# Optimization experiments

Measured on AMD Instinct MI355X. Metric: run time of the kernel, lower is better.

The kernel has to match this reference:

```python
import jax, jax.numpy as jnp
import numpy as np

# ---- static problem constants ----
B, N, L = 8, 256, 15.0          # molecules, atoms per molecule, cubic cell length (Angstrom)
DL, SIGMA = 1.5, 1.0            # Ewald k-space spacing and Gaussian smearing width
ELEMENTS = np.array([1, 6, 7, 8])
NORM_FACTOR = (1.0 / 90.0474) ** 0.5
TWO_PI = 2.0 * np.pi
KSQ_MAX = (TWO_PI / DL) ** 2
NMAX = int(np.ceil(L / DL))     # 10 -> (2*10+1)^3 = 9261 k-vectors
_g = np.arange(-NMAX, NMAX + 1)
K_GRID = jnp.asarray(np.stack(np.meshgrid(_g, _g, _g, indexing='ij'), -1)
                     .reshape(-1, 3).astype(np.float32))  # [K,3] integer k indices
_zmap = np.full(int(ELEMENTS.max()) + 1, -1)
for _i, _z in enumerate(ELEMENTS):
    _zmap[_z] = _i
Z_INDEX_MAP = jnp.asarray(_zmap)


def setup_inputs() -> dict:
    key = jax.random.key(0)
    k1, k2, k3, k4 = jax.random.split(key, 4)
    positions = jax.random.uniform(k1, (B * N, 3), jnp.float32) * L
    cell = jnp.tile((L * jnp.eye(3, dtype=jnp.float32))[None], (B, 1, 1))
    chi = jax.random.normal(k2, (B * N,), jnp.float32)
    idx = jax.random.randint(k3, (B * N,), 0, len(ELEMENTS))
    atomic_numbers = jnp.asarray(ELEMENTS)[idx]
    batch = jnp.repeat(jnp.arange(B), N)
    J_raw = jax.random.uniform(k4, (len(ELEMENTS),), jnp.float32, 0.5, 1.5)
    system_charge = jnp.zeros((B,), jnp.float32)
    return dict(positions=positions, cell=cell, chi=chi, J_raw=J_raw,
                system_charge=system_charge, atomic_numbers=atomic_numbers, batch=batch)


def _a_matrix(r, cell):
    """Reciprocal-space Ewald interaction matrix A (energy = 0.5 q^T A q), one molecule."""
    recip = TWO_PI * jnp.linalg.inv(cell).T            # rows: reciprocal lattice vectors
    k = K_GRID @ recip                                 # [K,3]
    k2 = jnp.sum(k * k, axis=-1)                       # [K]
    valid = (k2 > 1e-10) & (k2 < KSQ_MAX)
    f = jnp.where(valid, jnp.exp(-0.5 * SIGMA * SIGMA * k2) / jnp.maximum(k2, 1e-10), 0.0)
    vol = jnp.abs(jnp.linalg.det(cell))
    kr = r @ k.T                                       # [N,K]
    c, s = jnp.cos(kr), jnp.sin(kr)
    # A_ij = (4*pi/V) sum_k f(k) cos(k.(r_i - r_j))
    A = (2.0 * TWO_PI / vol) * ((c * f) @ c.T + (s * f) @ s.T)
    # remove Gaussian self-interaction: E_self = -sum_i q_i^2 / (sigma*sqrt(2*pi))
    A = A - (2.0 / (SIGMA * np.sqrt(TWO_PI))) * jnp.eye(N, dtype=r.dtype)
    return A


def _solve_qeq(A, chi_m, J_i, Q):
    """Charge-equilibration with Lagrange multiplier for total-charge constraint."""
    coeffs = jnp.ones((N + 1, N + 1), A.dtype)
    coeffs = coeffs.at[:N, :N].set(A + jnp.diag(J_i))
    coeffs = coeffs.at[N, N].set(0.0)
    rhs = jnp.concatenate([-chi_m, (Q / NORM_FACTOR)[None].astype(A.dtype)])
    sol = jnp.linalg.solve(coeffs, rhs)
    q = sol[:N]
    e = 0.5 * q @ (A @ q)
    return q, e


def reference(positions, cell, chi, J_raw, system_charge, atomic_numbers, batch):
    r = positions.reshape(B, N, 3)
    chi_b = chi.reshape(B, N)
    J_elem = jnp.square(J_raw)
    J_i = J_elem[Z_INDEX_MAP[atomic_numbers]].reshape(B, N)
    A = jax.vmap(_a_matrix)(r, cell)                   # [B,N,N]
    q, e = jax.vmap(_solve_qeq)(A, chi_b, J_i, system_charge)
    all_q_eq = q.reshape(B * N, 1)
    all_ewald = e                                      # [B]
    return all_q_eq, all_ewald
```

## Files before the change

### kernel.cpp

```cpp
#include <hip/hip_runtime.h>
#include <math.h>

#define NBATCH 8
#define NATOM  256
#define NP1    257
#define WROW   258
#define TOTALK 9261
#define KCAP   2560
#define KC     16
#define NB     16
#define UBW    244
#define BDF    768
#define BDB    256

#define TWO_PI_D 6.283185307179586
#define DIAG_SUB 0.7978845608028654

__device__ __constant__ int TI10[10] = {0,0,0,0,1,1,1,2,2,3};
__device__ __constant__ int TJ10[10] = {0,1,2,3,1,2,3,2,3,3};

struct GemmSh {
  int4   kn[KC];
  double kw[KC];
  double cI[KC][64], sI[KC][64];
  double cJ[KC][64], sJ[KC][64];
};

__device__ __forceinline__ void atomAddD(double* p, double v) {
#if defined(__has_builtin)
#if __has_builtin(__builtin_amdgcn_global_atomic_fadd_f64)
  __builtin_amdgcn_global_atomic_fadd_f64(p, v);
  return;
#endif
#endif
  unsigned long long* u = (unsigned long long*)p;
  unsigned long long old = *u, assumed;
  do {
    assumed = old;
    old = atomicCAS(u, assumed,
                    (unsigned long long)__double_as_longlong(
                        v + __longlong_as_double((long long)assumed)));
  } while (old != assumed);
}

__device__ __forceinline__ void classify2(const void* c0, const void* c1, const void* c2,
                                          const float*& chi, const int*& znum)
{
  const void* cands[3] = {c0, c1, c2};
  int got = 0;
  for (int i = 0; i < 3; i++) {
    unsigned uu = ((const unsigned*)cands[i])[0];
    if (uu == 0u) continue;
    else if (uu < 16u) { znum = (const int*)cands[i]; got |= 1; }
    else               { chi  = (const float*)cands[i]; got |= 2; }
  }
  if (got != 3) { chi = (const float*)c0; znum = (const int*)c1; }
}

__global__ __launch_bounds__(256) void zero_planes(
    double* __restrict__ P0g, int nplanes)
{
  const size_t npair = (size_t)nplanes * NBATCH * ((NP1*WROW) >> 1);
  double2* Z = (double2*)P0g;
  const double2 z = make_double2(0.0, 0.0);
  for (size_t i = (size_t)blockIdx.x*256 + threadIdx.x; i < npair;
       i += (size_t)gridDim.x*256)
    Z[i] = z;
}

__global__ __launch_bounds__(256) void prep(
    const float* __restrict__ pos, const float* __restrict__ cell,
    double2* __restrict__ Tg, int4* __restrict__ klist,
    double* __restrict__ kw, int* __restrict__ kcount,
    const void* __restrict__ c0, const void* __restrict__ c1, const void* __restrict__ c2,
    const float* __restrict__ syschg,
    double* __restrict__ P0g, int nplanes)
{
  const int b = blockIdx.x;
  const int tid = threadIdx.x;
  __shared__ double ivs[9];
  __shared__ double prefs;
  __shared__ int cnt;
  if (tid == 0) {
    double c[9];
#pragma unroll
    for (int i = 0; i < 9; i++) c[i] = (double)cell[b*9+i];
    double det = c[0]*(c[4]*c[8]-c[5]*c[7]) - c[1]*(c[3]*c[8]-c[5]*c[6])
               + c[2]*(c[3]*c[7]-c[4]*c[6]);
    double idet = 1.0/det;
    ivs[0]=(c[4]*c[8]-c[5]*c[7])*idet; ivs[1]=(c[2]*c[7]-c[1]*c[8])*idet; ivs[2]=(c[1]*c[5]-c[2]*c[4])*idet;
    ivs[3]=(c[5]*c[6]-c[3]*c[8])*idet; ivs[4]=(c[0]*c[8]-c[2]*c[6])*idet; ivs[5]=(c[2]*c[3]-c[0]*c[5])*idet;
    ivs[6]=(c[3]*c[7]-c[4]*c[6])*idet; ivs[7]=(c[1]*c[6]-c[0]*c[7])*idet; ivs[8]=(c[0]*c[4]-c[1]*c[3])*idet;
    prefs = 2.0*TWO_PI_D/fabs(det);
    cnt = 0;
  }
  __syncthreads();
  {
    const int a = tid;
    double x = (double)pos[((size_t)b*NATOM+a)*3+0];
    double y = (double)pos[((size_t)b*NATOM+a)*3+1];
    double z = (double)pos[((size_t)b*NATOM+a)*3+2];
    double u[3];
    u[0] = TWO_PI_D*(ivs[0]*x + ivs[3]*y + ivs[6]*z);
    u[1] = TWO_PI_D*(ivs[1]*x + ivs[4]*y + ivs[7]*z);
    u[2] = TWO_PI_D*(ivs[2]*x + ivs[5]*y + ivs[8]*z);
#pragma unroll
    for (int d = 0; d < 3; d++) {
      double2* T = Tg + (size_t)((b*3 + d)*21)*256;
      double c1 = cos(u[d]);
      double s1 = sin(u[d]);
      T[10*256 + a] = make_double2(1.0, 0.0);
      T[11*256 + a] = make_double2(c1,  s1);
      T[ 9*256 + a] = make_double2(c1, -s1);
      double cp = c1, sp = s1;
      for (int n = 2; n <= 10; n++) {
        double cn = cp*c1 - sp*s1;
        double sn = sp*c1 + cp*s1;
        cp = cn; sp = sn;
        T[(10+n)*256 + a] = make_double2(cp,  sp);
        T[(10-n)*256 + a] = make_double2(cp, -sp);
      }
    }
  }
  const double ksqmax = (TWO_PI_D/1.5)*(TWO_PI_D/1.5);
  for (int m = tid; m < TOTALK; m += 256) {
    int n1 = m/441 - 10;
    int n2 = (m/21)%21 - 10;
    int n3 = m%21 - 10;
    bool half = (n1 > 0) || (n1 == 0 && (n2 > 0 || (n2 == 0 && n3 > 0)));
    if (!half) continue;
    double d1 = n1, d2 = n2, d3 = n3;
    double kx = TWO_PI_D*(ivs[0]*d1 + ivs[1]*d2 + ivs[2]*d3);
    double ky = TWO_PI_D*(ivs[3]*d1 + ivs[4]*d2 + ivs[5]*d3);
    double kz = TWO_PI_D*(ivs[6]*d1 + ivs[7]*d2 + ivs[8]*d3);
    double k2 = kx*kx + ky*ky + kz*kz;
    if (k2 > 1e-10 && k2 < ksqmax) {
      double w = 2.0 * prefs * exp(-0.5*k2) / k2;
      int slot = atomicAdd(&cnt, 1);
      klist[b*KCAP + slot] = make_int4(n1, n2, n3, 0);
      kw[b*KCAP + slot] = w;
    }
  }
  __syncthreads();
  {
    const float* chi = nullptr; const int* znum = nullptr;
    classify2(c0, c1, c2, chi, znum);
    double* P0b = P0g + (size_t)b*NP1*WROW;
    for (int i = tid; i < NATOM; i += 256) {
      P0b[(size_t)NATOM*WROW + i] = 1.0;
      P0b[(size_t)i*WROW + NATOM] = 1.0;
      P0b[(size_t)i*WROW + 257]   = -(double)chi[b*NATOM + i];
    }
    if (tid == 0) {
      P0b[(size_t)NATOM*WROW + NATOM] = 0.0;
      P0b[(size_t)NATOM*WROW + 257]   = (double)syschg[b]*sqrt(90.0474);
      kcount[b] = cnt;
    }
  }
}

__device__ void gemm_tile(int b, int ti, int tj, int tid,
                          const double2* __restrict__ Tg,
                          const int4* __restrict__ klist,
                          const double* __restrict__ kw, int ks, int ke,
                          double* __restrict__ Ab, bool mirror, GemmSh& S)
{
  const int tx = tid & 15, ty = tid >> 4;
  const int ro = ty << 2, co = tx << 2;
  double acc[16];
#pragma unroll
  for (int i = 0; i < 16; i++) acc[i] = 0.0;

  for (int k0 = ks; k0 < ke; k0 += KC) {
    if (tid < KC) {
      int kk = k0 + tid;
      if (kk < ke) { S.kn[tid] = klist[b*KCAP + kk]; S.kw[tid] = kw[b*KCAP + kk]; }
      else         { S.kn[tid] = make_int4(0,0,0,0); S.kw[tid] = 0.0; }
    }
    __syncthreads();
#pragma unroll
    for (int p = 0; p < 8; p++) {
      int idx = p*256 + tid;
      int a    = idx & 63;
      int kk   = (idx >> 6) & (KC-1);
      int side = idx >> 10;
      int atom = ((side == 0) ? ti : tj) + a;
      int4 nn = S.kn[kk];
      double2 t1 = Tg[(size_t)((b*3+0)*21 + (nn.x+10))*256 + atom];
      double2 t2 = Tg[(size_t)((b*3+1)*21 + (nn.y+10))*256 + atom];
      double2 t3 = Tg[(size_t)((b*3+2)*21 + (nn.z+10))*256 + atom];
      double ex = t1.x*t2.x - t1.y*t2.y;
      double ey = t1.x*t2.y + t1.y*t2.x;
      double cx = ex*t3.x - ey*t3.y;
      double cy = ex*t3.y + ey*t3.x;
      if (side == 0) { double w = S.kw[kk]; S.cI[kk][a] = w*cx; S.sI[kk][a] = w*cy; }
      else           { S.cJ[kk][a] = cx; S.sJ[kk][a] = cy; }
    }
    __syncthreads();
#pragma unroll
    for (int kk = 0; kk < KC; kk++) {
      double ci[4], si[4], cj[4], sj[4];
#pragma unroll
      for (int r = 0; r < 2; r++) {
        double2 v0 = *(const double2*)&S.cI[kk][ro + 2*r];
        ci[2*r] = v0.x; ci[2*r+1] = v0.y;
        double2 v1 = *(const double2*)&S.sI[kk][ro + 2*r];
        si[2*r] = v1.x; si[2*r+1] = v1.y;
        double2 v2 = *(const double2*)&S.cJ[kk][co + 2*r];
        cj[2*r] = v2.x; cj[2*r+1] = v2.y;
        double2 v3 = *(const double2*)&S.sJ[kk][co + 2*r];
        sj[2*r] = v3.x; sj[2*r+1] = v3.y;
      }
#pragma unroll
      for (int r = 0; r < 4; r++)
#pragma unroll
        for (int c = 0; c < 4; c++)
          acc[r*4+c] += ci[r]*cj[c] + si[r]*sj[c];
    }
    __syncthreads();
  }
#pragma unroll
  for (int r = 0; r < 4; r++) {
#pragma unroll
    for (int c = 0; c < 4; c++) {
      int gr = ti + ro + r, gc = tj + co + c;
      double v = acc[r*4+c];
      atomAddD(&Ab[(size_t)gr*WROW + gc], v);
      if (mirror && ti != tj) atomAddD(&Ab[(size_t)gc*WROW + gr], v);
    }
  }
}

__device__ __forceinline__ double* plane_sel(double* P0, double* P1, double* P2, int s) {
  return (s == 0) ? P0 : ((s == 1) ? P1 : P2);
}

__global__ __launch_bounds__(256) void build_A_gemm(
    const double2* __restrict__ Tg, const int4* __restrict__ klist,
    const double* __restrict__ kw, const int* __restrict__ kcount,
    double* __restrict__ P0g, double* __restrict__ P1g, double* __restrict__ P2g,
    int nplanes)
{
  __shared__ GemmSh S;
  const int nseg = 2*nplanes;
  const int u = blockIdx.x;
  const int seg = u / 80;
  const int r = u - seg*80;
  const int b = r / 10;
  const int t = r - b*10;
  const int s = (seg < nplanes) ? seg : (seg - nplanes);
  const int cnt = kcount[b];
  const int ks = (int)((long long)cnt * seg / nseg);
  const int ke = (int)((long long)cnt * (seg+1) / nseg);
  double* Ab = plane_sel(P0g, P1g, P2g, s) + (size_t)b*NP1*WROW;
  gemm_tile(b, TI10[t]*64, TJ10[t]*64, threadIdx.x, Tg, klist, kw, ks, ke, Ab, true, S);
}

__global__ __launch_bounds__(BDF, 2) void solve_factor(
    double* __restrict__ P0g, const double* __restrict__ P1g, const double* __restrict__ P2g,
    int nplanes,
    const void* __restrict__ c0, const void* __restrict__ c1, const void* __restrict__ c2,
    const float* __restrict__ Jraw)
{
  const int b = blockIdx.x;
  const int tid = threadIdx.x;
  double* Pb = P0g + (size_t)b*NP1*WROW;
  const double* Qb = P1g + (size_t)b*NP1*WROW;
  const double* Rb = P2g + (size_t)b*NP1*WROW;
  const bool two   = (nplanes > 1);
  const bool three = (nplanes > 2);

  __shared__ __align__(16) double pan[NP1+4][NB+2];
  __shared__ double dnv[NB];
  __shared__ __align__(16) double Ub[NB][UBW];

  const float* chi = nullptr; const int* znum = nullptr;
  classify2(c0, c1, c2, chi, znum);
  const float J0 = Jraw[0], J1 = Jraw[1], J2 = Jraw[2], J3 = Jraw[3];

  for (int p0 = 0; p0 < NP1; p0 += NB) {
    const int pw  = (NB < NP1 - p0) ? NB : (NP1 - p0);
    const int nr  = NP1 - p0;
    const int nrt = nr - pw;
    const int tc0 = p0 + pw;
    const int tc  = WROW - tc0;
    const bool first = (p0 == 0);
    for (int idx = tid; idx < nr*pw; idx += BDF) {
      int r, c;
      if (pw == NB) { r = idx >> 4; c = idx & 15; } else { r = idx; c = 0; }
      double v;
      if (first) {
        size_t a = (size_t)r*WROW + c;
        v = Pb[a];
        if (two)   v += Qb[a];
        if (three) v += Rb[a];
        if (r == c) {
          int z = znum[b*NATOM + r];
          float Jr = (z == 1) ? J0 : (z == 6) ? J1 : (z == 7) ? J2 : J3;
          v += (double)Jr*(double)Jr - DIAG_SUB;
        }
      } else {
        v = Pb[(size_t)(p0+r)*WROW + p0 + c];
      }
      pan[r][c] = v;
    }
    __syncthreads();
    if (pw == NB) {
      if (tid < NB) {
        double v[NB];
#pragma unroll
        for (int c = 0; c < NB; c++) v[c] = pan[tid][c];
#pragma unroll
        for (int c = 0; c < NB; c++) {
          double piv = __shfl(v[c], c);
          double dinv = 1.0 / piv;
          if (tid == c) dnv[c] = dinv;
          double f = v[c] * dinv;
#pragma unroll
          for (int cc = 0; cc < NB; cc++) {
            if (cc > c) {
              double ucc = __shfl(v[cc], c);
              if (tid > c) v[cc] -= f * ucc;
            }
          }
          if (tid > c) v[c] = f;
        }
#pragma unroll
        for (int c = 0; c < NB; c++) pan[tid][c] = v[c];
      }
    }
    __syncthreads();
    if (pw == NB) {
      if (tid < nrt) {
        const int r = NB + tid;
        double w[NB];
#pragma unroll
        for (int c = 0; c < NB; c++) w[c] = pan[r][c];
#pragma unroll
        for (int c = 0; c < NB; c++) {
          double s = w[c];
#pragma unroll
          for (int c2 = 0; c2 < NB; c2++) if (c2 < c) s -= w[c2] * pan[c2][c];
          w[c] = s * dnv[c];
        }
#pragma unroll
        for (int c = 0; c < NB; c++) pan[r][c] = w[c];
      } else if (tid >= 256 && tid < 256 + tc) {
        const int j = tc0 + (tid - 256);
        double v[NB];
#pragma unroll
        for (int c = 0; c < NB; c++) {
          size_t a = (size_t)(p0+c)*WROW + j;
          double t = Pb[a];
          if (first) {
            if (two)   t += Qb[a];
            if (three) t += Rb[a];
          }
          v[c] = t;
        }
#pragma unroll
        for (int c = 0; c < NB; c++)
#pragma unroll
          for (int r2 = 0; r2 < NB; r2++) if (r2 > c) v[r2] -= pan[r2][c]*v[c];
#pragma unroll
        for (int c = 0; c < NB; c++) {
          Pb[(size_t)(p0+c)*WROW + j] = v[c];
          Ub[c][tid - 256] = v[c];
        }
      } else {
        const int nh = (256 - nrt) + (BDF - 256 - tc);
        int hid = (tid < 256) ? (tid - nrt) : ((256 - nrt) + (tid - 256 - tc));
        for (int idx = hid; idx < NB*NB; idx += nh) {
          int r2 = idx >> 4, c2 = idx & 15;
          Pb[(size_t)(p0+r2)*WROW + p0 + c2] = pan[r2][c2];
        }
      }
    } else {
      if (tid == 0) Pb[(size_t)p0*WROW + p0] = pan[0][0];
    }
    __syncthreads();
    if (pw == NB) {
      const int jp   = tid & 127;
      const int rowg = tid >> 7;
      const int j0 = 2*jp;
      if (j0 < tc && nrt > 0) {
        double va[NB], vb[NB];
#pragma unroll
        for (int c = 0; c < NB; c++) {
          double2 u = *(const double2*)&Ub[c][j0];
          va[c] = u.x; vb[c] = u.y;
        }
        auto loadrow = [&](int rr, double2& x0, double2& x1) {
          x0 = make_double2(0.0, 0.0); x1 = x0;
          if (rr < nrt) {
            const int row0 = tc0 + rr;
            const size_t ad = (size_t)row0*WROW + tc0 + j0;
            x0 = *(const double2*)&Pb[ad];
            if (rr + 1 < nrt) x1 = *(const double2*)&Pb[ad + WROW];
            if (first) {
              if (two) {
                double2 q0 = *(const double2*)&Qb[ad]; x0.x += q0.x; x0.y += q0.y;
                if (rr + 1 < nrt) { double2 q1 = *(const double2*)&Qb[ad + WROW]; x1.x += q1.x; x1.y += q1.y; }
              }
              if (three) {
                double2 r0v = *(const double2*)&Rb[ad]; x0.x += r0v.x; x0.y += r0v.y;
                if (rr + 1 < nrt) { double2 r1v = *(const double2*)&Rb[ad + WROW]; x1.x += r1v.x; x1.y += r1v.y; }
              }
              if (rr == j0) {
                if (row0 < NATOM) {
                  int z = znum[b*NATOM + row0];
                  float Jr = (z == 1) ? J0 : (z == 6) ? J1 : (z == 7) ? J2 : J3;
                  x0.x += (double)Jr*(double)Jr - DIAG_SUB;
                }
                if (rr + 1 < nrt && row0 + 1 < NATOM) {
                  int z = znum[b*NATOM + row0 + 1];
                  float Jr = (z == 1) ? J0 : (z == 6) ? J1 : (z == 7) ? J2 : J3;
                  x1.y += (double)Jr*(double)Jr - DIAG_SUB;
                }
              }
            }
          }
        };
        int rr = 2*rowg;
        double2 a0, a1;
        loadrow(rr, a0, a1);
        while (rr < nrt) {
          const int rn = rr + 12;
          double2 n0, n1;
          loadrow(rn, n0, n1);
          const double* pr0 = pan[NB + rr];
          const double* pr1 = pan[NB + rr + 1];
#pragma unroll
          for (int m = 0; m < NB/2; m++) {
            double2 l0 = *(const double2*)&pr0[2*m];
            double2 l1 = *(const double2*)&pr1[2*m];
            a0.x -= l0.x*va[2*m] + l0.y*va[2*m+1];
            a0.y -= l0.x*vb[2*m] + l0.y*vb[2*m+1];
            a1.x -= l1.x*va[2*m] + l1.y*va[2*m+1];
            a1.y -= l1.x*vb[2*m] + l1.y*vb[2*m+1];
          }
          const size_t ad = (size_t)(tc0+rr)*WROW + tc0 + j0;
          *(double2*)&Pb[ad] = a0;
          if (rr + 1 < nrt) *(double2*)&Pb[ad + WROW] = a1;
          a0 = n0; a1 = n1;
          rr = rn;
        }
      }
    }
    __syncthreads();
  }
}

__global__ __launch_bounds__(BDB) void solve_back(
    double* __restrict__ P0g,
    const void* __restrict__ c0, const void* __restrict__ c1, const void* __restrict__ c2,
    const float* __restrict__ Jraw, const float* __restrict__ syschg,
    float* __restrict__ out)
{
  const int b = blockIdx.x;
  const int tid = threadIdx.x;
  double* Pb = P0g + (size_t)b*NP1*WROW;

  __shared__ double panb[NB][NB+1];
  __shared__ double xs[NP1];
  __shared__ double red[BDB];

  const float* chi = nullptr; const int* znum = nullptr;
  classify2(c0, c1, c2, chi, znum);
  const double rhsN = (double)syschg[b] * sqrt(90.0474);
  const float J0 = Jraw[0], J1 = Jraw[1], J2 = Jraw[2], J3 = Jraw[3];

  for (int r = tid; r < NP1; r += BDB) xs[r] = Pb[(size_t)r*WROW + 257];
  __syncthreads();
  for (int pb0 = 256; pb0 >= 0; pb0 -= NB) {
    const int w = (pb0 == 256) ? 1 : NB;
    if (w == NB) {
      {
        const int i = tid >> 4, c = tid & 15;
        panb[i][c] = Pb[(size_t)(pb0+i)*WROW + pb0 + c];
      }
      __syncthreads();
      if (tid < NB) {
        double u[NB];
#pragma unroll
        for (int c = 0; c < NB; c++) u[c] = panb[tid][c];
        double y  = xs[pb0 + tid];
        double di = 1.0 / panb[tid][tid];
        double xr = 0.0;
#pragma unroll
        for (int i = NB-1; i >= 0; i--) {
          double xi = y * di;
          xi = __shfl(xi, i);
          if (tid == i) xr = xi;
          if (tid < i)  y -= u[i] * xi;
        }
        xs[pb0 + tid] = xr;
      }
    } else {
      if (tid == 0) xs[256] = xs[256] / Pb[(size_t)256*WROW + 256];
    }
    __syncthreads();
    if (tid < pb0) {
      const double* rowp = &Pb[(size_t)tid*WROW + pb0];
      double s = 0.0;
      for (int c = 0; c < w; c++) s += rowp[c]*xs[pb0+c];
      xs[tid] -= s;
    }
    __syncthreads();
  }

  out[b*NATOM + tid] = (float)xs[tid];
  const double lam = xs[NATOM];
  double q  = xs[tid];
  double ch = (double)chi[b*NATOM + tid];
  int z = znum[b*NATOM + tid];
  float Jr = (z == 1) ? J0 : (z == 6) ? J1 : (z == 7) ? J2 : J3;
  red[tid] = q*ch + (double)Jr*(double)Jr*q*q;
  __syncthreads();
  for (int st = BDB/2; st > 0; st >>= 1) {
    if (tid < st) red[tid] += red[tid + st];
    __syncthreads();
  }
  if (tid == 0)
    out[NBATCH*NATOM + b] = (float)(-0.5*(red[0] + lam*rhsN));
}

extern "C" void kernel_launch(void* const* d_in, const int* in_sizes, int n_in,
                              void* d_out, int out_size, void* d_ws, size_t ws_size,
                              hipStream_t stream)
{
  int iPos=-1, iCell=-1, iJ=-1, iQ=-1, cand[3]={-1,-1,-1}, nc=0;
  for (int i = 0; i < n_in; i++) {
    int s = in_sizes[i];
    if      (s == 6144) iPos  = i;
    else if (s == 72)   iCell = i;
    else if (s == 4)    iJ    = i;
    else if (s == 8)    iQ    = i;
    else if (s == 2048 && nc < 3) cand[nc++] = i;
  }
  if (!(iPos>=0 && iCell>=0 && iJ>=0 && iQ>=0 && nc>=2)) {
    iPos=iCell=iJ=iQ=-1; nc=0; cand[0]=cand[1]=cand[2]=-1;
    for (int i = 0; i < n_in; i++) {
      int s = in_sizes[i];
      if      (s == 24576) iPos  = i;
      else if (s == 288)   iCell = i;
      else if (s == 16)    iJ    = i;
      else if (s == 32)    iQ    = i;
      else if (s == 8192 && nc < 3) cand[nc++] = i;
    }
  }
  if (!(iPos>=0 && iCell>=0 && iJ>=0 && iQ>=0 && nc>=2)) {
    iPos=0; iCell=1; iJ=3; iQ=4; cand[0]=2; cand[1]=5; cand[2]=6; nc=3;
  }
  if (nc == 2) cand[2] = cand[1];

  const float* pos  = (const float*)d_in[iPos];
  const float* cell = (const float*)d_in[iCell];
  const float* Jraw = (const float*)d_in[iJ];
  const float* sysq = (const float*)d_in[iQ];
  const void*  c0   = d_in[cand[0]];
  const void*  c1   = d_in[cand[1]];
  const void*  c2   = d_in[cand[2]];
  float* out = (float*)d_out;

  const size_t planeB = (size_t)NBATCH*NP1*WROW*sizeof(double);
  const size_t tgB = 2064384, klB = 327680, kwB = 163840;
  const size_t trigAll = tgB + klB + kwB + 64;
  int nplanes = (ws_size >= 3*planeB + trigAll) ? 3 :
                ((ws_size >= 2*planeB + trigAll) ? 2 : 1);

  char* ws = (char*)d_ws;
  double*  P0g = (double*)ws;
  double*  P1g = (nplanes > 1) ? (double*)(ws + planeB)   : P0g;
  double*  P2g = (nplanes > 2) ? (double*)(ws + 2*planeB) : P1g;
  char* trigBase = ws + (size_t)nplanes*planeB;
  double2* Tg     = (double2*)trigBase;
  int4*    klist  = (int4*)  (trigBase + tgB);
  double*  kwa    = (double*)(trigBase + tgB + klB);
  int*     kcount = (int*)   (trigBase + tgB + klB + kwB);

  hipLaunchKernelGGL(zero_planes,  dim3(512),           dim3(256), 0, stream,
                     P0g, nplanes);
  hipLaunchKernelGGL(prep,         dim3(NBATCH),        dim3(256), 0, stream,
                     pos, cell, Tg, klist, kwa, kcount, c0, c1, c2, sysq,
                     P0g, nplanes);
  hipLaunchKernelGGL(build_A_gemm, dim3(160*nplanes),   dim3(256), 0, stream,
                     Tg, klist, kwa, kcount, P0g, P1g, P2g, nplanes);
  hipLaunchKernelGGL(solve_factor, dim3(NBATCH),        dim3(BDF), 0, stream,
                     P0g, P1g, P2g, nplanes, c0, c1, c2, Jraw);
  hipLaunchKernelGGL(solve_back,   dim3(NBATCH),        dim3(BDB), 0, stream,
                     P0g, c0, c1, c2, Jraw, sysq, out);
}
```

Before: 625.6 us.

## Split blocked LU factor across two cooperating blocks per molecule with flag sync

New measurement: 591.1 us. 1.06x faster.

```diff
diff --git a/kernel.cpp b/kernel.cpp
--- a/kernel.cpp
+++ b/kernel.cpp
@@ -9,9 +9,11 @@
 #define KCAP   2560
 #define KC     16
 #define NB     16
-#define UBW    244
+#define UBW    124
 #define BDF    768
 #define BDB    256
+#define FLAGOFF 2528
+#define SLOTMAX 2500
 
 #define TWO_PI_D 6.283185307179586
 #define DIAG_SUB 0.7978845608028654
@@ -58,8 +60,12 @@
 }
 
 __global__ __launch_bounds__(256) void zero_planes(
-    double* __restrict__ P0g, int nplanes)
-{
+    double* __restrict__ P0g, int4* __restrict__ klist, int nplanes)
+{
+  if (blockIdx.x == 0 && threadIdx.x < 256) {
+    const int b = threadIdx.x >> 5, s = threadIdx.x & 31;
+    klist[(size_t)b*KCAP + FLAGOFF + s] = make_int4(0, 0, 0, 0);
+  }
   const size_t npair = (size_t)nplanes * NBATCH * ((NP1*WROW) >> 1);
   double2* Z = (double2*)P0g;
   const double2 z = make_double2(0.0, 0.0);
@@ -137,8 +143,10 @@
     if (k2 > 1e-10 && k2 < ksqmax) {
       double w = 2.0 * prefs * exp(-0.5*k2) / k2;
       int slot = atomicAdd(&cnt, 1);
-      klist[b*KCAP + slot] = make_int4(n1, n2, n3, 0);
-      kw[b*KCAP + slot] = w;
+      if (slot < SLOTMAX) {
+        klist[b*KCAP + slot] = make_int4(n1, n2, n3, 0);
+        kw[b*KCAP + slot] = w;
+      }
     }
   }
   __syncthreads();
@@ -154,7 +162,7 @@
     if (tid == 0) {
       P0b[(size_t)NATOM*WROW + NATOM] = 0.0;
       P0b[(size_t)NATOM*WROW + 257]   = (double)syschg[b]*sqrt(90.0474);
-      kcount[b] = cnt;
+      kcount[b] = (cnt < SLOTMAX) ? cnt : SLOTMAX;
     }
   }
 }
@@ -260,15 +268,20 @@
     double* __restrict__ P0g, const double* __restrict__ P1g, const double* __restrict__ P2g,
     int nplanes,
     const void* __restrict__ c0, const void* __restrict__ c1, const void* __restrict__ c2,
-    const float* __restrict__ Jraw)
-{
-  const int b = blockIdx.x;
+    const float* __restrict__ Jraw,
+    int4* __restrict__ klist, double* __restrict__ U11g)
+{
+  const int b = blockIdx.x >> 1;
+  const int h = blockIdx.x & 1;
   const int tid = threadIdx.x;
   double* Pb = P0g + (size_t)b*NP1*WROW;
   const double* Qb = P1g + (size_t)b*NP1*WROW;
   const double* Rb = P2g + (size_t)b*NP1*WROW;
   const bool two   = (nplanes > 1);
   const bool three = (nplanes > 2);
+  int* FA = (int*)(klist + (size_t)b*KCAP + FLAGOFF);
+  int* FB = FA + 32;
+  double* U11b = U11g + (size_t)b*17*256;
 
   __shared__ __align__(16) double pan[NP1+4][NB+2];
   __shared__ double dnv[NB];
@@ -278,13 +291,26 @@
   classify2(c0, c1, c2, chi, znum);
   const float J0 = Jraw[0], J1 = Jraw[1], J2 = Jraw[2], J3 = Jraw[3];
 
-  for (int p0 = 0; p0 < NP1; p0 += NB) {
+  int p = 0;
+  for (int p0 = 0; p0 < NP1; p0 += NB, p++) {
     const int pw  = (NB < NP1 - p0) ? NB : (NP1 - p0);
     const int nr  = NP1 - p0;
     const int nrt = nr - pw;
     const int tc0 = p0 + pw;
     const int tc  = WROW - tc0;
     const bool first = (p0 == 0);
+    int leftCols = (tc >= 4) ? (((tc >> 1) + 1) & ~1) : tc;
+    const int clo = (h == 0) ? tc0 : tc0 + leftCols;
+    const int chiC = (h == 0) ? tc0 + leftCols : tc0 + tc;
+    const int ownCols = chiC - clo;
+    if (p > 0) {
+      if (tid == 0) {
+        while (atomicAdd(&FA[p-1], 0) == 0) __builtin_amdgcn_s_sleep(2);
+        while (atomicAdd(&FB[p-1], 0) == 0) __builtin_amdgcn_s_sleep(2);
+        __threadfence();
+      }
+      __syncthreads();
+    }
     for (int idx = tid; idx < nr*pw; idx += BDF) {
       int r, c;
       if (pw == NB) { r = idx >> 4; c = idx & 15; } else { r = idx; c = 0; }
@@ -345,8 +371,8 @@
         }
 #pragma unroll
         for (int c = 0; c < NB; c++) pan[r][c] = w[c];
-      } else if (tid >= 256 && tid < 256 + tc) {
-        const int j = tc0 + (tid - 256);
+      } else if (tid >= 256 && tid < 256 + ownCols) {
+        const int j = clo + (tid - 256);
         double v[NB];
 #pragma unroll
         for (int c = 0; c < NB; c++) {
@@ -367,34 +393,30 @@
           Pb[(size_t)(p0+c)*WROW + j] = v[c];
           Ub[c][tid - 256] = v[c];
         }
-      } else {
-        const int nh = (256 - nrt) + (BDF - 256 - tc);
-        int hid = (tid < 256) ? (tid - nrt) : ((256 - nrt) + (tid - 256 - tc));
-        for (int idx = hid; idx < NB*NB; idx += nh) {
-          int r2 = idx >> 4, c2 = idx & 15;
-          Pb[(size_t)(p0+r2)*WROW + p0 + c2] = pan[r2][c2];
-        }
+      } else if (h == 0 && tid >= 512) {
+        const int idx = tid - 512;
+        U11b[p*256 + idx] = pan[idx >> 4][idx & 15];
       }
     } else {
-      if (tid == 0) Pb[(size_t)p0*WROW + p0] = pan[0][0];
-    }
-    __syncthreads();
-    if (pw == NB) {
-      const int jp   = tid & 127;
-      const int rowg = tid >> 7;
-      const int j0 = 2*jp;
-      if (j0 < tc && nrt > 0) {
+      if (h == 0 && tid == 0) U11b[16*256] = pan[0][0];
+    }
+    __syncthreads();
+    if (pw == NB && ownCols > 0 && nrt > 0) {
+      const int jp   = tid & 63;
+      const int rowg = tid >> 6;
+      if (clo + 2*jp < chiC) {
+        const int jrel = (clo - tc0) + 2*jp;
         double va[NB], vb[NB];
 #pragma unroll
         for (int c = 0; c < NB; c++) {
-          double2 u = *(const double2*)&Ub[c][j0];
+          double2 u = *(const double2*)&Ub[c][2*jp];
           va[c] = u.x; vb[c] = u.y;
         }
         auto loadrow = [&](int rr, double2& x0, double2& x1) {
           x0 = make_double2(0.0, 0.0); x1 = x0;
           if (rr < nrt) {
             const int row0 = tc0 + rr;
-            const size_t ad = (size_t)row0*WROW + tc0 + j0;
+            const size_t ad = (size_t)row0*WROW + tc0 + jrel;
             x0 = *(const double2*)&Pb[ad];
             if (rr + 1 < nrt) x1 = *(const double2*)&Pb[ad + WROW];
             if (first) {
@@ -406,14 +428,15 @@
                 double2 r0v = *(const double2*)&Rb[ad]; x0.x += r0v.x; x0.y += r0v.y;
                 if (rr + 1 < nrt) { double2 r1v = *(const double2*)&Rb[ad + WROW]; x1.x += r1v.x; x1.y += r1v.y; }
               }
-              if (rr == j0) {
-                if (row0 < NATOM) {
-                  int z = znum[b*NATOM + row0];
+              if (rr == jrel) {
+                const int row0g = tc0 + rr;
+                if (row0g < NATOM) {
+                  int z = znum[b*NATOM + row0g];
                   float Jr = (z == 1) ? J0 : (z == 6) ? J1 : (z == 7) ? J2 : J3;
                   x0.x += (double)Jr*(double)Jr - DIAG_SUB;
                 }
-                if (rr + 1 < nrt && row0 + 1 < NATOM) {
-                  int z = znum[b*NATOM + row0 + 1];
+                if (rr + 1 < nrt && row0g + 1 < NATOM) {
+                  int z = znum[b*NATOM + row0g + 1];
                   float Jr = (z == 1) ? J0 : (z == 6) ? J1 : (z == 7) ? J2 : J3;
                   x1.y += (double)Jr*(double)Jr - DIAG_SUB;
                 }
@@ -425,7 +448,7 @@
         double2 a0, a1;
         loadrow(rr, a0, a1);
         while (rr < nrt) {
-          const int rn = rr + 12;
+          const int rn = rr + 24;
           double2 n0, n1;
           loadrow(rn, n0, n1);
           const double* pr0 = pan[NB + rr];
@@ -439,7 +462,7 @@
             a1.x -= l1.x*va[2*m] + l1.y*va[2*m+1];
             a1.y -= l1.x*vb[2*m] + l1.y*vb[2*m+1];
           }
-          const size_t ad = (size_t)(tc0+rr)*WROW + tc0 + j0;
+          const size_t ad = (size_t)(tc0+rr)*WROW + tc0 + jrel;
           *(double2*)&Pb[ad] = a0;
           if (rr + 1 < nrt) *(double2*)&Pb[ad + WROW] = a1;
           a0 = n0; a1 = n1;
@@ -448,11 +471,16 @@
       }
     }
     __syncthreads();
+    if (pw == NB && tid == 0) {
+      __threadfence();
+      if (h == 0) atomicExch(&FA[p], 1);
+      else        atomicExch(&FB[p], 1);
+    }
   }
 }
 
 __global__ __launch_bounds__(BDB) void solve_back(
-    double* __restrict__ P0g,
+    double* __restrict__ P0g, const double* __restrict__ U11g,
     const void* __restrict__ c0, const void* __restrict__ c1, const void* __restrict__ c2,
     const float* __restrict__ Jraw, const float* __restrict__ syschg,
     float* __restrict__ out)
@@ -460,6 +488,7 @@
   const int b = blockIdx.x;
   const int tid = threadIdx.x;
   double* Pb = P0g + (size_t)b*NP1*WROW;
+  const double* U11b = U11g + (size_t)b*17*256;
 
   __shared__ double panb[NB][NB+1];
   __shared__ double xs[NP1];
@@ -477,7 +506,7 @@
     if (w == NB) {
       {
         const int i = tid >> 4, c = tid & 15;
-        panb[i][c] = Pb[(size_t)(pb0+i)*WROW + pb0 + c];
+        panb[i][c] = U11b[(pb0 >> 4)*256 + i*16 + c];
       }
       __syncthreads();
       if (tid < NB) {
@@ -497,7 +526,7 @@
         xs[pb0 + tid] = xr;
       }
     } else {
-      if (tid == 0) xs[256] = xs[256] / Pb[(size_t)256*WROW + 256];
+      if (tid == 0) xs[256] = xs[256] / U11b[16*256];
     }
     __syncthreads();
     if (tid < pb0) {
@@ -578,16 +607,17 @@
   int4*    klist  = (int4*)  (trigBase + tgB);
   double*  kwa    = (double*)(trigBase + tgB + klB);
   int*     kcount = (int*)   (trigBase + tgB + klB + kwB);
+  double*  U11g   = (double*)trigBase;
 
   hipLaunchKernelGGL(zero_planes,  dim3(512),           dim3(256), 0, stream,
-                     P0g, nplanes);
+                     P0g, klist, nplanes);
   hipLaunchKernelGGL(prep,         dim3(NBATCH),        dim3(256), 0, stream,
                      pos, cell, Tg, klist, kwa, kcount, c0, c1, c2, sysq,
                      P0g, nplanes);
   hipLaunchKernelGGL(build_A_gemm, dim3(160*nplanes),   dim3(256), 0, stream,
                      Tg, klist, kwa, kcount, P0g, P1g, P2g, nplanes);
-  hipLaunchKernelGGL(solve_factor, dim3(NBATCH),        dim3(BDF), 0, stream,
-                     P0g, P1g, P2g, nplanes, c0, c1, c2, Jraw);
+  hipLaunchKernelGGL(solve_factor, dim3(2*NBATCH),      dim3(BDF), 0, stream,
+                     P0g, P1g, P2g, nplanes, c0, c1, c2, Jraw, klist, U11g);
   hipLaunchKernelGGL(solve_back,   dim3(NBATCH),        dim3(BDB), 0, stream,
-                     P0g, c0, c1, c2, Jraw, sysq, out);
-}
+                     P0g, U11g, c0, c1, c2, Jraw, sysq, out);
+}
```
